# Performance work log

Hardware: AMD Instinct MI355X
Metric: run time of the kernel (lower is better)

The kernel has to match this reference:

```python
import jax, jax.numpy as jnp
import numpy as np

L, B, E, H, HID = 2048, 4, 512, 8, 2048
HD = E // H


def setup_inputs() -> dict:
    key = jax.random.key(0)
    ks = jax.random.split(key, 6)
    s = 0.02
    x = jax.random.normal(ks[0], (L, B, E), jnp.float32)
    in_proj_w = jax.random.normal(ks[1], (3 * E, E), jnp.float32) * s
    in_proj_b = jnp.zeros((3 * E,), jnp.float32)
    out_w = jax.random.normal(ks[2], (E, E), jnp.float32) * s
    out_b = jnp.zeros((E,), jnp.float32)
    w1 = jax.random.normal(ks[3], (HID, E), jnp.float32) * s  # torch Linear: (out, in)
    b1 = jnp.zeros((HID,), jnp.float32)
    w2 = jax.random.normal(ks[4], (E, HID), jnp.float32) * s
    b2 = jnp.zeros((E,), jnp.float32)
    ln_g = jnp.ones((E,), jnp.float32)
    ln_b = jnp.zeros((E,), jnp.float32)
    return {"x": x, "in_proj_w": in_proj_w, "in_proj_b": in_proj_b,
            "out_w": out_w, "out_b": out_b, "w1": w1, "b1": b1,
            "w2": w2, "b2": b2, "ln_g": ln_g, "ln_b": ln_b}


def _pos_encoding(S, Emb, dtype):
    # even i: sin((t+1) * 10000^(-i/E)); odd i: cos((t+1) * 10000^(-(i+1)/E))
    t = jnp.arange(S, dtype=dtype)[:, None]
    i = jnp.arange(Emb, dtype=dtype)[None, :]
    even = jnp.sin((t + 1.0) * jnp.power(10000.0, -i / Emb))
    odd = jnp.cos((t + 1.0) * jnp.power(10000.0, -(i + 1.0) / Emb))
    return jnp.where(jnp.arange(Emb)[None, :] % 2 == 0, even, odd)  # (S, Emb)


def _layernorm(x, g, b, eps=1e-5):
    mu = jnp.mean(x, axis=-1, keepdims=True)
    var = jnp.mean(jnp.square(x - mu), axis=-1, keepdims=True)
    return (x - mu) * jax.lax.rsqrt(var + eps) * g + b


def _mha(x, in_proj_w, in_proj_b, out_w, out_b):
    # x: (L, B, E); self-attention, torch MultiheadAttention semantics
    qkv = jnp.einsum('lbe,fe->lbf', x, in_proj_w) + in_proj_b
    q, k, v = jnp.split(qkv, 3, axis=-1)
    q = q.reshape(L, B, H, HD)
    k = k.reshape(L, B, H, HD)
    v = v.reshape(L, B, H, HD)
    scores = jnp.einsum('lbhd,mbhd->bhlm', q, k) / np.sqrt(HD).astype(np.float32)
    attn = jax.nn.softmax(scores, axis=-1)
    o = jnp.einsum('bhlm,mbhd->lbhd', attn, v).reshape(L, B, E)
    return jnp.einsum('lbe,fe->lbf', o, out_w) + out_b


def reference(x, in_proj_w, in_proj_b, out_w, out_b, w1, b1, w2, b2, ln_g, ln_b):
    # positional encoding: varies along dim1, broadcasts along dim0 (as in source)
    pe = _pos_encoding(x.shape[1], x.shape[2], x.dtype)  # (B, E)
    x = x + pe[None, :, :]
    # Post-Norm path
    x = _layernorm(_mha(x, in_proj_w, in_proj_b, out_w, out_b) + x, ln_g, ln_b)
    h = jax.nn.gelu(jnp.einsum('lbe,he->lbh', x, w1) + b1, approximate=False)
    ff = jnp.einsum('lbh,eh->lbe', h, w2) + b2
    x = _layernorm(ff + x, ln_g, ln_b)
    return x
```

## Files before the change

kernel.cpp:

```cpp
#include <hip/hip_runtime.h>

typedef unsigned short u16;
typedef unsigned int   u32;
typedef u16  u16x2 __attribute__((ext_vector_type(2)));
typedef u16  u16x4 __attribute__((ext_vector_type(4)));
typedef u16  u16x8 __attribute__((ext_vector_type(8)));
typedef short s8v  __attribute__((ext_vector_type(8)));
typedef short s4v  __attribute__((ext_vector_type(4)));
typedef float f4v  __attribute__((ext_vector_type(4)));
typedef u32  u32x2 __attribute__((ext_vector_type(2)));
typedef u32  u32x4 __attribute__((ext_vector_type(4)));

#define L_SEQ 2048
#define B_SZ  4
#define E_DIM 512
#define H_CNT 8
#define HD    64
#define HID   2048
#define M_ROWS (L_SEQ * B_SZ)
#define QSCALE 0.18033688011112042f

__device__ __forceinline__ u16 f2b(float f) {
    unsigned u = __builtin_bit_cast(unsigned, f);
    u += 0x7fffu + ((u >> 16) & 1u);
    return (u16)(u >> 16);
}
__device__ __forceinline__ float b2f(u16 u) {
    u32 x = ((u32)u) << 16; return __builtin_bit_cast(float, x);
}
#if defined(__has_builtin)
#if __has_builtin(__builtin_amdgcn_cvt_pk_bf16_f32)
#define HAVE_PK_BF16 1
#endif
#endif
__device__ __forceinline__ u32 pk_trunc(float a, float b) {
#ifdef HAVE_PK_BF16
    typedef __bf16 bf2 __attribute__((ext_vector_type(2)));
    bf2 r = __builtin_amdgcn_cvt_pk_bf16_f32(a, b);
    return __builtin_bit_cast(u32, r);
#else
    u32 ua = __builtin_bit_cast(u32, a), ub = __builtin_bit_cast(u32, b);
    return (ua >> 16) | (ub & 0xffff0000u);
#endif
}
__device__ __forceinline__ void gload_lds16(const u16* g, u16* l) {
    __builtin_amdgcn_global_load_lds((__attribute__((address_space(1))) void*)(u16*)g,
                                     (__attribute__((address_space(3))) void*)l, 16, 0, 0);
}
__device__ __forceinline__ float gelu_f(float v) {
    float y2 = v * (1.5957691216f + 0.0713548576f * v * v);
    return v / (1.0f + __expf(-y2));
}

__global__ __launch_bounds__(256) void pe_tab_k(float* __restrict__ pet) {
    int i = blockIdx.x * 256 + threadIdx.x;
    int e = i & (E_DIM - 1);
    float t = (float)(i >> 9) + 1.0f;
    int ee = (e & 1) ? (e + 1) : e;
    float w = exp2f((-(float)ee / 512.0f) * 13.287712379549449f);
    pet[i] = (e & 1) ? cosf(t * w) : sinf(t * w);
}

__global__ __launch_bounds__(256) void pe_add_k(const float* __restrict__ x,
                                                const float* __restrict__ pet,
                                                u16* __restrict__ xpb) {
    int idx = (blockIdx.x * 256 + threadIdx.x) * 4;
    f4v v = *(const f4v*)(x + idx);
    f4v p = *(const f4v*)(pet + (idx & 2047));
    u16x4 o;
#pragma unroll
    for (int i = 0; i < 4; ++i) o[i] = f2b(v[i] + p[i]);
    *(u16x4*)(xpb + idx) = o;
}

__global__ __launch_bounds__(256) void conv4_k(const float* __restrict__ s1, u16* __restrict__ d1, int n1,
                                               const float* __restrict__ s2, u16* __restrict__ d2, int n2,
                                               const float* __restrict__ s3, u16* __restrict__ d3, int n3,
                                               const float* __restrict__ s4, u16* __restrict__ d4) {
    int o = (blockIdx.x * 256 + threadIdx.x) * 4;
    const float* s; u16* d;
    if (o < n1) { s = s1; d = d1; }
    else { o -= n1;
        if (o < n2) { s = s2; d = d2; }
        else { o -= n2;
            if (o < n3) { s = s3; d = d3; }
            else { o -= n3; s = s4; d = d4; } } }
    f4v v = *(const f4v*)(s + o);
    u16x4 q;
#pragma unroll
    for (int i = 0; i < 4; ++i) q[i] = f2b(v[i]);
    *(u16x4*)(d + o) = q;
}

template <int NP, bool WRITEF, bool WRITEB>
__global__ __launch_bounds__(256)
void ln_c(const u16* __restrict__ p0, const u16* __restrict__ p1,
          const u16* __restrict__ p2, const u16* __restrict__ p3,
          const float* __restrict__ bias, const u16* __restrict__ resid,
          const float* __restrict__ gw, const float* __restrict__ bw,
          float* __restrict__ outF, u16* __restrict__ outB) {
    int wave = threadIdx.x >> 6, lane = threadIdx.x & 63;
    size_t row = (size_t)blockIdx.x * 4 + wave;
    size_t off = row * E_DIM + lane * 8;
    u16x8 rv = *(const u16x8*)(resid + off);
    f4v a, b;
#pragma unroll
    for (int i = 0; i < 4; ++i) { a[i] = b2f(rv[i]); b[i] = b2f(rv[i + 4]); }
    a += *(const f4v*)(bias + lane * 8);
    b += *(const f4v*)(bias + lane * 8 + 4);
    const u16* ps[4] = {p0, p1, p2, p3};
#pragma unroll
    for (int z = 0; z < NP; ++z) {
        u16x8 t = *(const u16x8*)(ps[z] + off);
#pragma unroll
        for (int i = 0; i < 4; ++i) { a[i] += b2f(t[i]); b[i] += b2f(t[i + 4]); }
    }
    float s = (a[0] + a[1]) + (a[2] + a[3]) + (b[0] + b[1]) + (b[2] + b[3]);
#pragma unroll
    for (int o = 1; o < 64; o <<= 1) s += __shfl_xor(s, o, 64);
    float mu = s * (1.0f / E_DIM);
    float q = 0.f;
#pragma unroll
    for (int i = 0; i < 4; ++i) { float d = a[i] - mu; q += d * d; }
#pragma unroll
    for (int i = 0; i < 4; ++i) { float d = b[i] - mu; q += d * d; }
#pragma unroll
    for (int o = 1; o < 64; o <<= 1) q += __shfl_xor(q, o, 64);
    float rstd = rsqrtf(q * (1.0f / E_DIM) + 1e-5f);
    f4v g0 = *(const f4v*)(gw + lane * 8), g1 = *(const f4v*)(gw + lane * 8 + 4);
    f4v w0 = *(const f4v*)(bw + lane * 8), w1 = *(const f4v*)(bw + lane * 8 + 4);
    f4v y0, y1;
#pragma unroll
    for (int i = 0; i < 4; ++i) { y0[i] = (a[i] - mu) * rstd * g0[i] + w0[i];
                                  y1[i] = (b[i] - mu) * rstd * g1[i] + w1[i]; }
    if (WRITEF) {
        *(f4v*)(outF + off)     = y0;
        *(f4v*)(outF + off + 4) = y1;
    }
    if (WRITEB) {
        u16x8 o;
#pragma unroll
        for (int i = 0; i < 4; ++i) { o[i] = f2b(y0[i]); o[i + 4] = f2b(y1[i]); }
        *(u16x8*)(outB + off) = o;
    }
}

__global__ __launch_bounds__(256) void transpose_v_k(const u16* __restrict__ vb,
                                                     u16* __restrict__ vt) {
    __shared__ __align__(16) u16 T[64 * 66];
    int t = threadIdx.x;
    int lt = blockIdx.x, bh = blockIdx.y;
    const u16* src = vb + (size_t)bh * (L_SEQ * HD) + (size_t)lt * 64 * HD;
    int lr = t >> 2, d0 = (t & 3) * 16;
    s8v va = *(const s8v*)(src + lr * HD + d0);
    s8v vb8 = *(const s8v*)(src + lr * HD + d0 + 8);
#pragma unroll
    for (int c = 0; c < 4; ++c) {
        u16x2 p0; p0[0] = (u16)va[c * 2]; p0[1] = (u16)va[c * 2 + 1];
        u16x2 p1; p1[0] = (u16)vb8[c * 2]; p1[1] = (u16)vb8[c * 2 + 1];
        *(u16x2*)(&T[lr * 66 + d0 + c * 2])     = p0;
        *(u16x2*)(&T[lr * 66 + d0 + 8 + c * 2]) = p1;
    }
    __syncthreads();
    int d = t >> 2, l0 = (t & 3) * 16;
    u16 tmp[16];
#pragma unroll
    for (int i = 0; i < 16; ++i) tmp[i] = T[(l0 + i) * 66 + d];
    u16* dst = vt + (size_t)bh * (L_SEQ * HD) + (size_t)d * L_SEQ + lt * 64 + l0;
    u16x8 o0, o1;
#pragma unroll
    for (int i = 0; i < 8; ++i) { o0[i] = tmp[i]; o1[i] = tmp[8 + i]; }
    *(u16x8*)dst       = o0;
    *(u16x8*)(dst + 8) = o1;
}

template <int MODE, int NT>
__global__ __launch_bounds__(256, 4)
void gemm_bt(const u16* __restrict__ A, const u16* __restrict__ Bw,
             const float* __restrict__ bias, int M, int N, int K,
             u16* __restrict__ outB,
             u16* __restrict__ oq, u16* __restrict__ okk, u16* __restrict__ ov) {
    __shared__ __align__(16) u16 As[2][128 * 32];
    __shared__ __align__(16) u16 Bs[2][128 * 32];
    const int tid = threadIdx.x;
    const int wave = tid >> 6, lane = tid & 63;
    const int col = lane & 15, quad = lane >> 4;
    const int n = blockIdx.x;
    const int xcd = n & 7, loc = n >> 3;
    const int mpx = (M / 128) >> 3;
    const int bm = (xcd * mpx + loc / NT) * 128;
    const int bn = (loc % NT) * 128;
    const int wm = (wave >> 1) * 64, wn = (wave & 1) * 64;
    f4v acc[4][4] = {};
    const int srow = wave * 16 + (lane >> 2);
    const int soff = (lane & 3) * 8;
    const u16* Ag = A + (size_t)(bm + srow) * K + soff;
    const u16* Bg = Bw + (size_t)(bn + srow) * K + soff;
    const int wo = wave * 512;
    gload_lds16(Ag,                  &As[0][wo]);
    gload_lds16(Ag + (size_t)64 * K, &As[0][wo + 2048]);
    gload_lds16(Bg,                  &Bs[0][wo]);
    gload_lds16(Bg + (size_t)64 * K, &Bs[0][wo + 2048]);
    const int nit = K >> 5;
    for (int t = 0; t < nit; ++t) {
        const int cur = t & 1, nxt = cur ^ 1;
        __syncthreads();
        if (t + 1 < nit) {
            const int kc = (t + 1) * 32;
            gload_lds16(Ag + kc,                  &As[nxt][wo]);
            gload_lds16(Ag + (size_t)64 * K + kc, &As[nxt][wo + 2048]);
            gload_lds16(Bg + kc,                  &Bs[nxt][wo]);
            gload_lds16(Bg + (size_t)64 * K + kc, &Bs[nxt][wo + 2048]);
        }
        s8v af[4], bf[4];
#pragma unroll
        for (int i = 0; i < 4; ++i) af[i] = *(const s8v*)(&As[cur][(wm + i * 16 + col) * 32 + quad * 8]);
#pragma unroll
        for (int j = 0; j < 4; ++j) bf[j] = *(const s8v*)(&Bs[cur][(wn + j * 16 + col) * 32 + quad * 8]);
#pragma unroll
        for (int i = 0; i < 4; ++i)
#pragma unroll
            for (int j = 0; j < 4; ++j)
                acc[i][j] = __builtin_amdgcn_mfma_f32_16x16x32_bf16(af[i], bf[j], acc[i][j], 0, 0, 0);
    }
#pragma unroll
    for (int j = 0; j < 4; ++j) {
        int gn = bn + wn + j * 16 + col;
        float bv = bias[gn];
        int which = gn >> 9, hh = (gn >> 6) & 7, d = gn & 63;
        u16* dst = (MODE == 0) ? ((which == 0) ? oq : ((which == 1) ? okk : ov)) : outB;
        float qs = (MODE == 0 && which == 0) ? QSCALE : 1.0f;
#pragma unroll
        for (int i = 0; i < 4; ++i) {
            int gm0 = bm + wm + i * 16 + quad * 4;
#pragma unroll
            for (int r = 0; r < 4; ++r) {
                float v = acc[i][j][r] + bv;
                int m = gm0 + r;
                if (MODE == 2) {
                    outB[(size_t)m * N + gn] = f2b(gelu_f(v));
                } else {
                    int l = m >> 2, bb = m & 3;
                    dst[((size_t)(bb * H_CNT + hh) * L_SEQ + l) * HD + d] = f2b(v * qs);
                }
            }
        }
    }
}

__global__ __launch_bounds__(256, 4)
void gemm_ks(const u16* __restrict__ A, const u16* __restrict__ Bw,
             int N, int K, int Kper,
             u16* __restrict__ q0, u16* __restrict__ q1) {
    __shared__ __align__(16) u16 As[2][128 * 32];
    __shared__ __align__(16) u16 Bs[2][128 * 32];
    const int tid = threadIdx.x;
    const int wave = tid >> 6, lane = tid & 63;
    const int col = lane & 15, quad = lane >> 4;
    const int n = blockIdx.x;
    const int xcd = n & 7, loc = n >> 3;
    const int bn = (loc & 3) * 128;
    const int bm = (xcd * 8 + ((loc >> 2) & 7)) * 128;
    const int kz = loc >> 5;
    u16* pz = kz ? q1 : q0;
    const int wm = (wave >> 1) * 64, wn = (wave & 1) * 64;
    f4v acc[4][4] = {};
    const int srow = wave * 16 + (lane >> 2);
    const int soff = (lane & 3) * 8;
    const u16* Ag = A + (size_t)(bm + srow) * K + kz * Kper + soff;
    const u16* Bg = Bw + (size_t)(bn + srow) * K + kz * Kper + soff;
    const int wo = wave * 512;
    gload_lds16(Ag,                  &As[0][wo]);
    gload_lds16(Ag + (size_t)64 * K, &As[0][wo + 2048]);
    gload_lds16(Bg,                  &Bs[0][wo]);
    gload_lds16(Bg + (size_t)64 * K, &Bs[0][wo + 2048]);
    const int nit = Kper >> 5;
    for (int t = 0; t < nit; ++t) {
        const int cur = t & 1, nxt = cur ^ 1;
        __syncthreads();
        if (t + 1 < nit) {
            const int kc = (t + 1) * 32;
            gload_lds16(Ag + kc,                  &As[nxt][wo]);
            gload_lds16(Ag + (size_t)64 * K + kc, &As[nxt][wo + 2048]);
            gload_lds16(Bg + kc,                  &Bs[nxt][wo]);
            gload_lds16(Bg + (size_t)64 * K + kc, &Bs[nxt][wo + 2048]);
        }
        s8v af[4], bf[4];
#pragma unroll
        for (int i = 0; i < 4; ++i) af[i] = *(const s8v*)(&As[cur][(wm + i * 16 + col) * 32 + quad * 8]);
#pragma unroll
        for (int j = 0; j < 4; ++j) bf[j] = *(const s8v*)(&Bs[cur][(wn + j * 16 + col) * 32 + quad * 8]);
#pragma unroll
        for (int i = 0; i < 4; ++i)
#pragma unroll
            for (int j = 0; j < 4; ++j)
                acc[i][j] = __builtin_amdgcn_mfma_f32_16x16x32_bf16(af[i], bf[j], acc[i][j], 0, 0, 0);
    }
#pragma unroll
    for (int j = 0; j < 4; ++j) {
        int gn = bn + wn + j * 16 + col;
#pragma unroll
        for (int i = 0; i < 4; ++i) {
            int m0 = bm + wm + i * 16 + quad * 4;
#pragma unroll
            for (int r = 0; r < 4; ++r)
                pz[(size_t)(m0 + r) * N + gn] = f2b(acc[i][j][r]);
        }
    }
}

__global__ __launch_bounds__(256, 4)
void attn_k(const u16* __restrict__ qg, const u16* __restrict__ kg,
            const u16* __restrict__ vtg,
            u16* __restrict__ po0, u16* __restrict__ po1,
            u16* __restrict__ po2, u16* __restrict__ po3, float* __restrict__ lbuf) {
    __shared__ __align__(16) u16 Ks[2][2][64 * 32];
    __shared__ __align__(16) u16 Vs[2][2][64 * 32];
    const int tid = threadIdx.x;
    const int wave = tid >> 6, lane = tid & 63;
    const int col = lane & 15, quad = lane >> 4;
    const int qc = blockIdx.x, kz = blockIdx.y, bh = blockIdx.z;
    const size_t base = (size_t)bh * (L_SEQ * HD);
    s8v qf[2][2];
#pragma unroll
    for (int t = 0; t < 2; ++t) {
        const int qrow = qc * 128 + wave * 32 + t * 16 + col;
#pragma unroll
        for (int hh = 0; hh < 2; ++hh)
            qf[t][hh] = *(const s8v*)(qg + base + (size_t)qrow * HD + hh * 32 + quad * 8);
    }
    f4v oa[2][4] = {};
    f4v la[2] = {};
    const s8v vones8 = {0x3F80, 0x3F80, 0x3F80, 0x3F80, 0x3F80, 0x3F80, 0x3F80, 0x3F80};
    const int h = wave & 1, r0 = (wave >> 1) * 16;
    const int srow = lane >> 2, c = lane & 3;
    const int cp = c ^ ((srow >> 1) & 3);
    const int sig = ((srow >> 2) << 3) + ((r0 >> 4) << 2) + (srow & 3);
    const u16* Kg = kg + base + (size_t)sig * HD + h * 32 + cp * 8;
    const u16* Vg = vtg + base + (size_t)(r0 + srow) * L_SEQ + h * 32 + cp * 8;
    const int kt0 = kz * 8;
    {
        const int kv0 = kt0 * 64;
        gload_lds16(Kg + (size_t)kv0 * HD,         &Ks[0][h][r0 * 32]);
        gload_lds16(Kg + (size_t)(kv0 + 32) * HD,  &Ks[0][h][(r0 + 32) * 32]);
        gload_lds16(Vg + kv0,                      &Vs[0][h][r0 * 32]);
        gload_lds16(Vg + kv0 + (size_t)32 * L_SEQ, &Vs[0][h][(r0 + 32) * 32]);
    }
    const int perm = (col >> 1) & 3;
#pragma unroll
    for (int it = 0; it < 8; ++it) {
        const int cur = it & 1, nxt = cur ^ 1;
        __syncthreads();
        if (it + 1 < 8) {
            const int kv0 = (kt0 + it + 1) * 64;
            gload_lds16(Kg + (size_t)kv0 * HD,         &Ks[nxt][h][r0 * 32]);
            gload_lds16(Kg + (size_t)(kv0 + 32) * HD,  &Ks[nxt][h][(r0 + 32) * 32]);
            gload_lds16(Vg + kv0,                      &Vs[nxt][h][r0 * 32]);
            gload_lds16(Vg + kv0 + (size_t)32 * L_SEQ, &Vs[nxt][h][(r0 + 32) * 32]);
        }
        f4v st[2][4];
#pragma unroll
        for (int j = 0; j < 4; ++j) {
            s8v k0 = *(const s8v*)(&Ks[cur][0][(j * 16 + col) * 32 + ((quad ^ perm) * 8)]);
            s8v k1 = *(const s8v*)(&Ks[cur][1][(j * 16 + col) * 32 + ((quad ^ perm) * 8)]);
#pragma unroll
            for (int t = 0; t < 2; ++t) {
                f4v z = {};
                z = __builtin_amdgcn_mfma_f32_16x16x32_bf16(k0, qf[t][0], z, 0, 0, 0);
                z = __builtin_amdgcn_mfma_f32_16x16x32_bf16(k1, qf[t][1], z, 0, 0, 0);
                st[t][j] = z;
            }
        }
        u32 pk[2][4][2];
#pragma unroll
        for (int t = 0; t < 2; ++t)
#pragma unroll
            for (int j = 0; j < 4; ++j) {
                f4v p;
#pragma unroll
                for (int r = 0; r < 4; ++r) p[r] = __builtin_amdgcn_exp2f(st[t][j][r]);
                pk[t][j][0] = pk_trunc(p[0], p[1]);
                pk[t][j][1] = pk_trunc(p[2], p[3]);
            }
#pragma unroll
        for (int c2 = 0; c2 < 2; ++c2) {
            s8v pf[2];
#pragma unroll
            for (int t = 0; t < 2; ++t) {
                u32x4 q4 = {pk[t][2 * c2][0], pk[t][2 * c2][1],
                            pk[t][2 * c2 + 1][0], pk[t][2 * c2 + 1][1]};
                pf[t] = __builtin_bit_cast(s8v, q4);
            }
#pragma unroll
            for (int dj = 0; dj < 4; ++dj) {
                s8v vf = *(const s8v*)(&Vs[cur][c2][(dj * 16 + col) * 32 + ((quad ^ perm) * 8)]);
#pragma unroll
                for (int t = 0; t < 2; ++t)
                    oa[t][dj] = __builtin_amdgcn_mfma_f32_16x16x32_bf16(pf[t], vf, oa[t][dj], 0, 0, 0);
            }
#pragma unroll
            for (int t = 0; t < 2; ++t)
                la[t] = __builtin_amdgcn_mfma_f32_16x16x32_bf16(pf[t], vones8, la[t], 0, 0, 0);
        }
    }
    if (col == 0) {
#pragma unroll
        for (int t = 0; t < 2; ++t)
#pragma unroll
            for (int r = 0; r < 4; ++r)
                lbuf[kz * 65536 + bh * 2048 + (qc * 128 + wave * 32 + t * 16 + quad * 4 + r)] = la[t][r];
    }
    u16* pg = (kz == 0) ? po0 : (kz == 1) ? po1 : (kz == 2) ? po2 : po3;
    const int b = bh >> 3, hd = bh & 7;
#pragma unroll
    for (int t = 0; t < 2; ++t)
#pragma unroll
        for (int r = 0; r < 4; ++r) {
            int lrow = qc * 128 + wave * 32 + t * 16 + quad * 4 + r;
            size_t mrow = (size_t)(lrow * 4 + b) * E_DIM + hd * HD;
#pragma unroll
            for (int dj = 0; dj < 4; ++dj)
                pg[mrow + dj * 16 + col] = f2b(oa[t][dj][r]);
        }
}

__global__ __launch_bounds__(256)
void combine_k(const u16* __restrict__ p0, const u16* __restrict__ p1,
               const u16* __restrict__ p2, const u16* __restrict__ p3,
               const float* __restrict__ lbuf, u16* __restrict__ out) {
    int idx8 = blockIdx.x * 256 + threadIdx.x;
    int m = idx8 >> 6;
    int e0 = (idx8 & 63) * 8;
    int b = m & 3, lrow = m >> 2, h = e0 >> 6;
    int li = (b * 8 + h) * 2048 + lrow;
    float inv = 1.0f / (lbuf[li] + lbuf[65536 + li] + lbuf[131072 + li] + lbuf[196608 + li]);
    size_t off = (size_t)m * E_DIM + e0;
    u16x8 a0 = *(const u16x8*)(p0 + off);
    u16x8 a1 = *(const u16x8*)(p1 + off);
    u16x8 a2 = *(const u16x8*)(p2 + off);
    u16x8 a3 = *(const u16x8*)(p3 + off);
    u16x8 o;
#pragma unroll
    for (int i = 0; i < 8; ++i)
        o[i] = f2b(((b2f(a0[i]) + b2f(a1[i])) + (b2f(a2[i]) + b2f(a3[i]))) * inv);
    *(u16x8*)(out + off) = o;
}

extern "C" void kernel_launch(void* const* d_in, const int* in_sizes, int n_in,
                              void* d_out, int out_size, void* d_ws, size_t ws_size,
                              hipStream_t stream) {
    const float* x     = (const float*)d_in[0];
    const float* w_qkv = (const float*)d_in[1];
    const float* b_qkv = (const float*)d_in[2];
    const float* w_out = (const float*)d_in[3];
    const float* b_out = (const float*)d_in[4];
    const float* w1    = (const float*)d_in[5];
    const float* b1    = (const float*)d_in[6];
    const float* w2    = (const float*)d_in[7];
    const float* b2    = (const float*)d_in[8];
    const float* ln_g  = (const float*)d_in[9];
    const float* ln_b  = (const float*)d_in[10];

    char* ws = (char*)d_ws;
    u16*   WQKV = (u16*)(ws + 0);
    u16*   WOUT = (u16*)(ws + 1572864);
    u16*   W1B  = (u16*)(ws + 2097152);
    u16*   W2B  = (u16*)(ws + 4194304);
    u16*   XPB  = (u16*)(ws + 6291456);
    u16*   QB   = (u16*)(ws + 14680064);
    u16*   KB   = (u16*)(ws + 23068672);
    u16*   VB   = (u16*)(ws + 31457280);
    u16*   VT   = (u16*)(ws + 39845888);
    u16*   AP0  = (u16*)(ws + 48234496);
    u16*   AP1  = (u16*)(ws + 56623104);
    u16*   AP2  = (u16*)(ws + 65011712);
    u16*   AP3  = (u16*)(ws + 73400320);
    float* LB   = (float*)(ws + 81788928);
    float* PET  = (float*)(ws + 82837504);
    u16*   OB   = VB;
    u16*   OP0  = (u16*)(ws + 48234496);
    u16*   OP1  = (u16*)(ws + 56623104);
    u16*   X3B  = QB;
    u16*   HB   = (u16*)(ws + 48234496);
    u16*   FP0  = XPB;
    u16*   FP1  = KB;

    pe_tab_k<<<8, 256, 0, stream>>>(PET);
    pe_add_k<<<4096, 256, 0, stream>>>(x, PET, XPB);
    conv4_k<<<3072, 256, 0, stream>>>(w_qkv, WQKV, 3 * E_DIM * E_DIM,
                                      w_out, WOUT, E_DIM * E_DIM,
                                      w1, W1B, HID * E_DIM,
                                      w2, W2B);
    gemm_bt<0, 12><<<768, 256, 0, stream>>>(XPB, WQKV, b_qkv, M_ROWS, 3 * E_DIM, E_DIM,
                                            nullptr, QB, KB, VB);
    transpose_v_k<<<dim3(32, 32), 256, 0, stream>>>(VB, VT);
    attn_k<<<dim3(16, 4, 32), 256, 0, stream>>>(QB, KB, VT, AP0, AP1, AP2, AP3, LB);
    combine_k<<<2048, 256, 0, stream>>>(AP0, AP1, AP2, AP3, LB, OB);
    gemm_ks<<<512, 256, 0, stream>>>(OB, WOUT, E_DIM, E_DIM, 256, OP0, OP1);
    ln_c<2, false, true><<<2048, 256, 0, stream>>>(OP0, OP1, nullptr, nullptr,
                                                   b_out, XPB, ln_g, ln_b, nullptr, X3B);
    gemm_bt<2, 16><<<1024, 256, 0, stream>>>(X3B, W1B, b1, M_ROWS, HID, E_DIM,
                                             HB, nullptr, nullptr, nullptr);
    gemm_ks<<<512, 256, 0, stream>>>(HB, W2B, E_DIM, HID, 1024, FP0, FP1);
    ln_c<2, true, false><<<2048, 256, 0, stream>>>(FP0, FP1, nullptr, nullptr,
                                                   b2, X3B, ln_g, ln_b, (float*)d_out, nullptr);
}
```

Measured before the change: 258.2 us.

## Drop split-K attention, process full key range per block and normalize in-kernel

Attention no longer splits the key dimension four ways with a separate combine kernel. Each block now loops over all 32 key tiles and normalizes its output in place using a fast reciprocal of the row sum. This removes the partial-output writes, the row-sum buffer and the combine launch. Blocks are also remapped so that heads are grouped per XCD for cache locality. In exchange the grid shrinks from 2048 to 512 blocks, which may reduce occupancy and latency hiding on the GPU.

```diff
diff --git a/kernel.cpp b/kernel.cpp
--- a/kernel.cpp
+++ b/kernel.cpp
@@ -6,7 +6,6 @@
 typedef u16  u16x4 __attribute__((ext_vector_type(4)));
 typedef u16  u16x8 __attribute__((ext_vector_type(8)));
 typedef short s8v  __attribute__((ext_vector_type(8)));
-typedef short s4v  __attribute__((ext_vector_type(4)));
 typedef float f4v  __attribute__((ext_vector_type(4)));
 typedef u32  u32x2 __attribute__((ext_vector_type(2)));
 typedef u32  u32x4 __attribute__((ext_vector_type(4)));
@@ -31,6 +30,9 @@
 #if defined(__has_builtin)
 #if __has_builtin(__builtin_amdgcn_cvt_pk_bf16_f32)
 #define HAVE_PK_BF16 1
+#endif
+#if __has_builtin(__builtin_amdgcn_rcpf)
+#define HAVE_RCPF 1
 #endif
 #endif
 __device__ __forceinline__ u32 pk_trunc(float a, float b) {
@@ -41,6 +43,13 @@
 #else
     u32 ua = __builtin_bit_cast(u32, a), ub = __builtin_bit_cast(u32, b);
     return (ua >> 16) | (ub & 0xffff0000u);
+#endif
+}
+__device__ __forceinline__ float frcp(float x) {
+#ifdef HAVE_RCPF
+    return __builtin_amdgcn_rcpf(x);
+#else
+    return 1.0f / x;
 #endif
 }
 __device__ __forceinline__ void gload_lds16(const u16* g, u16* l) {
@@ -311,15 +320,16 @@
 
 __global__ __launch_bounds__(256, 4)
 void attn_k(const u16* __restrict__ qg, const u16* __restrict__ kg,
-            const u16* __restrict__ vtg,
-            u16* __restrict__ po0, u16* __restrict__ po1,
-            u16* __restrict__ po2, u16* __restrict__ po3, float* __restrict__ lbuf) {
+            const u16* __restrict__ vtg, u16* __restrict__ og) {
     __shared__ __align__(16) u16 Ks[2][2][64 * 32];
     __shared__ __align__(16) u16 Vs[2][2][64 * 32];
     const int tid = threadIdx.x;
     const int wave = tid >> 6, lane = tid & 63;
     const int col = lane & 15, quad = lane >> 4;
-    const int qc = blockIdx.x, kz = blockIdx.y, bh = blockIdx.z;
+    const int flat = blockIdx.x;
+    const int xcd = flat & 7, loc = flat >> 3;
+    const int bh = xcd * 4 + (loc >> 4);
+    const int qc = loc & 15;
     const size_t base = (size_t)bh * (L_SEQ * HD);
     s8v qf[2][2];
 #pragma unroll
@@ -338,21 +348,18 @@
     const int sig = ((srow >> 2) << 3) + ((r0 >> 4) << 2) + (srow & 3);
     const u16* Kg = kg + base + (size_t)sig * HD + h * 32 + cp * 8;
     const u16* Vg = vtg + base + (size_t)(r0 + srow) * L_SEQ + h * 32 + cp * 8;
-    const int kt0 = kz * 8;
     {
-        const int kv0 = kt0 * 64;
-        gload_lds16(Kg + (size_t)kv0 * HD,         &Ks[0][h][r0 * 32]);
-        gload_lds16(Kg + (size_t)(kv0 + 32) * HD,  &Ks[0][h][(r0 + 32) * 32]);
-        gload_lds16(Vg + kv0,                      &Vs[0][h][r0 * 32]);
-        gload_lds16(Vg + kv0 + (size_t)32 * L_SEQ, &Vs[0][h][(r0 + 32) * 32]);
+        gload_lds16(Kg,                      &Ks[0][h][r0 * 32]);
+        gload_lds16(Kg + (size_t)32 * HD,    &Ks[0][h][(r0 + 32) * 32]);
+        gload_lds16(Vg,                      &Vs[0][h][r0 * 32]);
+        gload_lds16(Vg + (size_t)32 * L_SEQ, &Vs[0][h][(r0 + 32) * 32]);
     }
     const int perm = (col >> 1) & 3;
-#pragma unroll
-    for (int it = 0; it < 8; ++it) {
+    for (int it = 0; it < 32; ++it) {
         const int cur = it & 1, nxt = cur ^ 1;
         __syncthreads();
-        if (it + 1 < 8) {
-            const int kv0 = (kt0 + it + 1) * 64;
+        if (it + 1 < 32) {
+            const int kv0 = (it + 1) * 64;
             gload_lds16(Kg + (size_t)kv0 * HD,         &Ks[nxt][h][r0 * 32]);
             gload_lds16(Kg + (size_t)(kv0 + 32) * HD,  &Ks[nxt][h][(r0 + 32) * 32]);
             gload_lds16(Vg + kv0,                      &Vs[nxt][h][r0 * 32]);
@@ -403,47 +410,18 @@
                 la[t] = __builtin_amdgcn_mfma_f32_16x16x32_bf16(pf[t], vones8, la[t], 0, 0, 0);
         }
     }
-    if (col == 0) {
-#pragma unroll
-        for (int t = 0; t < 2; ++t)
-#pragma unroll
-            for (int r = 0; r < 4; ++r)
-                lbuf[kz * 65536 + bh * 2048 + (qc * 128 + wave * 32 + t * 16 + quad * 4 + r)] = la[t][r];
-    }
-    u16* pg = (kz == 0) ? po0 : (kz == 1) ? po1 : (kz == 2) ? po2 : po3;
     const int b = bh >> 3, hd = bh & 7;
 #pragma unroll
     for (int t = 0; t < 2; ++t)
 #pragma unroll
         for (int r = 0; r < 4; ++r) {
+            float inv = frcp(la[t][r]);
             int lrow = qc * 128 + wave * 32 + t * 16 + quad * 4 + r;
             size_t mrow = (size_t)(lrow * 4 + b) * E_DIM + hd * HD;
 #pragma unroll
             for (int dj = 0; dj < 4; ++dj)
-                pg[mrow + dj * 16 + col] = f2b(oa[t][dj][r]);
-        }
-}
-
-__global__ __launch_bounds__(256)
-void combine_k(const u16* __restrict__ p0, const u16* __restrict__ p1,
-               const u16* __restrict__ p2, const u16* __restrict__ p3,
-               const float* __restrict__ lbuf, u16* __restrict__ out) {
-    int idx8 = blockIdx.x * 256 + threadIdx.x;
-    int m = idx8 >> 6;
-    int e0 = (idx8 & 63) * 8;
-    int b = m & 3, lrow = m >> 2, h = e0 >> 6;
-    int li = (b * 8 + h) * 2048 + lrow;
-    float inv = 1.0f / (lbuf[li] + lbuf[65536 + li] + lbuf[131072 + li] + lbuf[196608 + li]);
-    size_t off = (size_t)m * E_DIM + e0;
-    u16x8 a0 = *(const u16x8*)(p0 + off);
-    u16x8 a1 = *(const u16x8*)(p1 + off);
-    u16x8 a2 = *(const u16x8*)(p2 + off);
-    u16x8 a3 = *(const u16x8*)(p3 + off);
-    u16x8 o;
-#pragma unroll
-    for (int i = 0; i < 8; ++i)
-        o[i] = f2b(((b2f(a0[i]) + b2f(a1[i])) + (b2f(a2[i]) + b2f(a3[i]))) * inv);
-    *(u16x8*)(out + off) = o;
+                og[mrow + dj * 16 + col] = f2b(oa[t][dj][r] * inv);
+        }
 }
 
 extern "C" void kernel_launch(void* const* d_in, const int* in_sizes, int n_in,
@@ -471,11 +449,6 @@
     u16*   KB   = (u16*)(ws + 23068672);
     u16*   VB   = (u16*)(ws + 31457280);
     u16*   VT   = (u16*)(ws + 39845888);
-    u16*   AP0  = (u16*)(ws + 48234496);
-    u16*   AP1  = (u16*)(ws + 56623104);
-    u16*   AP2  = (u16*)(ws + 65011712);
-    u16*   AP3  = (u16*)(ws + 73400320);
-    float* LB   = (float*)(ws + 81788928);
     float* PET  = (float*)(ws + 82837504);
     u16*   OB   = VB;
     u16*   OP0  = (u16*)(ws + 48234496);
@@ -494,8 +467,7 @@
     gemm_bt<0, 12><<<768, 256, 0, stream>>>(XPB, WQKV, b_qkv, M_ROWS, 3 * E_DIM, E_DIM,
                                             nullptr, QB, KB, VB);
     transpose_v_k<<<dim3(32, 32), 256, 0, stream>>>(VB, VT);
-    attn_k<<<dim3(16, 4, 32), 256, 0, stream>>>(QB, KB, VT, AP0, AP1, AP2, AP3, LB);
-    combine_k<<<2048, 256, 0, stream>>>(AP0, AP1, AP2, AP3, LB, OB);
+    attn_k<<<512, 256, 0, stream>>>(QB, KB, VT, OB);
     gemm_ks<<<512, 256, 0, stream>>>(OB, WOUT, E_DIM, E_DIM, 256, OP0, OP1);
     ln_c<2, false, true><<<2048, 256, 0, stream>>>(OP0, OP1, nullptr, nullptr,
                                                    b_out, XPB, ln_g, ln_b, nullptr, X3B);
```

After: 248.9 us. 3.6% less time.
